# Kernel tuning notes

Measured on AMD Instinct MI355X. Metric: run time of the kernel, lower is better.

The kernel has to match this reference:

```python
import jax, jax.numpy as jnp
import numpy as np

NUM_INSTANCES = 64  # instance ids in [0, 64); id 0 is background and excluded


def _variance_smooth_loss(variances, ins_labels, num_segments):
    # variances: [N, D] float, ins_labels: [N] int
    N, D = variances.shape
    ones = jnp.ones((N,), dtype=variances.dtype)
    counts = jax.ops.segment_sum(ones, ins_labels, num_segments=num_segments)          # [S]
    sums = jax.ops.segment_sum(variances, ins_labels, num_segments=num_segments)       # [S, D]
    safe_counts = jnp.maximum(counts, 1.0)
    means = sums / safe_counts[:, None]                                                # per-instance mean [S, D]
    diff = variances - means[ins_labels]                                               # gather means back [N, D]
    sq = jnp.sum(diff * diff, axis=1)                                                  # [N]
    # per-instance MSE = sum of squared diffs / (K_i * D), matching nn.MSELoss (mean reduction)
    per_ins = jax.ops.segment_sum(sq, ins_labels, num_segments=num_segments) / (safe_counts * D)
    valid = (counts > 0) & (jnp.arange(num_segments) != 0)                             # skip id 0 & absent ids
    return jnp.sum(jnp.where(valid, per_ins, jnp.zeros_like(per_ins)))


def setup_inputs() -> dict:
    key = jax.random.key(0)
    k1, k2 = jax.random.split(key)
    N, D = 4_000_000, 8
    variances = jax.random.normal(k1, (N, D), dtype=jnp.float32)
    ins_labels = jax.random.randint(k2, (N,), 0, NUM_INSTANCES, dtype=jnp.int32)
    return {"variances": variances, "ins_labels": ins_labels}


def reference(variances, ins_labels):
    return _variance_smooth_loss(variances, ins_labels, NUM_INSTANCES)
```

## Files before the change

### kernel.cpp

```cpp
#include <hip/hip_runtime.h>

#define NUM_INST 64
#define SLOT 12
#define BLOCK 256
#define NWAVES 4
#define GRID 1024

__global__ __launch_bounds__(BLOCK) void vsl_main(const float4* __restrict__ rows,
                                                  const int* __restrict__ labels,
                                                  float* __restrict__ gacc, int n) {
    __shared__ float lds[NWAVES][NUM_INST * SLOT];
    const int tid = threadIdx.x;
    const int w = tid >> 6;
    const int lane = tid & 63;

    float s0 = 0, s1 = 0, s2 = 0, s3 = 0, s4 = 0, s5 = 0, s6 = 0, s7 = 0;
    float ssq = 0, cntf = 0;

    float* slotbase = &lds[w][lane * SLOT];
    const int stride = GRID * BLOCK;

    for (int i = blockIdx.x * BLOCK + tid;; i += stride) {
        const bool valid = (i < n);
        const unsigned long long bv = __ballot(valid);
        if (!bv) break;

        int lbl = 0;
        float4 a = {0, 0, 0, 0}, b = {0, 0, 0, 0};
        if (valid) {
            lbl = labels[i];
            a = rows[2 * i];
            b = rows[2 * i + 1];
        }

        *(float4*)(slotbase) = a;
        *(float4*)(slotbase + 4) = b;

        unsigned long long m = bv;
#pragma unroll
        for (int bpos = 0; bpos < 6; ++bpos) {
            const unsigned long long bb = __ballot((lbl >> bpos) & 1);
            m &= ((lane >> bpos) & 1) ? bb : ~bb;
        }
        cntf += (float)__popcll(m);

        asm volatile("s_waitcnt lgkmcnt(0)" ::: "memory");

        while (m) {
            const int s = (int)__builtin_ctzll(m);
            m &= m - 1;
            const float* sp = &lds[w][s * SLOT];
            const float4 p = *(const float4*)sp;
            const float4 q = *(const float4*)(sp + 4);
            s0 += p.x; s1 += p.y; s2 += p.z; s3 += p.w;
            s4 += q.x; s5 += q.y; s6 += q.z; s7 += q.w;
            ssq += p.x * p.x + p.y * p.y + p.z * p.z + p.w * p.w +
                   q.x * q.x + q.y * q.y + q.z * q.z + q.w * q.w;
        }
    }

    float* fb = &lds[w][lane * SLOT];
    fb[0] = s0; fb[1] = s1; fb[2] = s2; fb[3] = s3;
    fb[4] = s4; fb[5] = s5; fb[6] = s6; fb[7] = s7;
    fb[8] = ssq; fb[9] = cntf;
    __syncthreads();

    for (int j = tid; j < NUM_INST * 10; j += BLOCK) {
        const int lbl = j / 10;
        const int st = j - lbl * 10;
        float v = 0;
#pragma unroll
        for (int ww = 0; ww < NWAVES; ++ww) v += lds[ww][lbl * SLOT + st];
        atomicAdd(&gacc[j], v);
    }
}

__global__ __launch_bounds__(64) void vsl_final(const float* __restrict__ gacc,
                                                float* __restrict__ out) {
    const int s = threadIdx.x;
    float val = 0.0f;
    const float* base = &gacc[s * 10];
    const float cnt = base[9];
    if (s != 0 && cnt > 0.0f) {
        const float ss = base[8];
        float m2 = 0.0f;
#pragma unroll
        for (int d = 0; d < 8; ++d) {
            const float sd = base[d];
            m2 += sd * sd;
        }
        val = (ss - m2 / cnt) / (cnt * 8.0f);
    }
#pragma unroll
    for (int off = 32; off > 0; off >>= 1) val += __shfl_down(val, off, 64);
    if (s == 0) out[0] = val;
}

extern "C" void kernel_launch(void* const* d_in, const int* in_sizes, int n_in,
                              void* d_out, int out_size, void* d_ws, size_t ws_size,
                              hipStream_t stream) {
    const float* variances = (const float*)d_in[0];
    const int* labels = (const int*)d_in[1];
    const int n = in_sizes[1];
    float* gacc = (float*)d_ws;

    hipMemsetAsync(d_ws, 0, NUM_INST * 10 * sizeof(float), stream);
    vsl_main<<<GRID, BLOCK, 0, stream>>>((const float4*)variances, labels, gacc, n);
    vsl_final<<<1, 64, 0, stream>>>(gacc, (float*)d_out);
}
```

Baseline: 211.6 us.

## Prefetch next rows, precompute squares per row, use packed FP32 math and divergent slot scan

The main loop now software-pipelines the global loads, issuing the next iteration's label and row loads before processing the current one. Each lane computes its own row's squared norm once with packed FMA and publishes it to LDS, so the gather loop only adds a scalar instead of recomputing eight squares. Accumulation uses v_pk_add_f32 on paired channels, the lane-mask scan uses per-lane 32-bit find-first-bit, and the grid grows to 1792 blocks. The prefetch raises register pressure, and the extra LDS slot plus the per-lane loop adds some complexity.

```diff
diff --git a/kernel.cpp b/kernel.cpp
--- a/kernel.cpp
+++ b/kernel.cpp
@@ -2,39 +2,63 @@
 
 #define NUM_INST 64
 #define SLOT 12
+#define NSLOT 65
 #define BLOCK 256
 #define NWAVES 4
-#define GRID 1024
+#define GRID 1792
 
-__global__ __launch_bounds__(BLOCK) void vsl_main(const float4* __restrict__ rows,
+typedef float f32x4 __attribute__((ext_vector_type(4)));
+typedef float f32x2 __attribute__((ext_vector_type(2)));
+
+__device__ __forceinline__ void pk_add(f32x2& acc, f32x2 v) {
+    asm("v_pk_add_f32 %0, %0, %1" : "+v"(acc) : "v"(v));
+}
+__device__ __forceinline__ void pk_fma_sq(f32x2& acc, f32x2 v) {
+    asm("v_pk_fma_f32 %0, %1, %1, %0" : "+v"(acc) : "v"(v));
+}
+
+__global__ __launch_bounds__(BLOCK) void vsl_main(const f32x4* __restrict__ rows,
                                                   const int* __restrict__ labels,
                                                   float* __restrict__ gacc, int n) {
-    __shared__ float lds[NWAVES][NUM_INST * SLOT];
+    __shared__ float lds[NWAVES][NSLOT * SLOT];
     const int tid = threadIdx.x;
     const int w = tid >> 6;
     const int lane = tid & 63;
+    float* const wbase = &lds[w][0];
 
-    float s0 = 0, s1 = 0, s2 = 0, s3 = 0, s4 = 0, s5 = 0, s6 = 0, s7 = 0;
+    if (lane < 9) wbase[64 * SLOT + lane] = 0.0f;
+
+    f32x2 acc01 = {0, 0}, acc23 = {0, 0}, acc45 = {0, 0}, acc67 = {0, 0};
     float ssq = 0, cntf = 0;
 
-    float* slotbase = &lds[w][lane * SLOT];
+    float* const pub = wbase + lane * SLOT;
     const int stride = GRID * BLOCK;
 
-    for (int i = blockIdx.x * BLOCK + tid;; i += stride) {
-        const bool valid = (i < n);
-        const unsigned long long bv = __ballot(valid);
-        if (!bv) break;
+    int i = blockIdx.x * BLOCK + tid;
+    bool valid = (i < n);
+    unsigned long long bv = __ballot(valid);
+    int lbl = 0;
+    f32x4 a = {0, 0, 0, 0}, b = {0, 0, 0, 0};
+    if (valid) { lbl = labels[i]; a = rows[2 * i]; b = rows[2 * i + 1]; }
 
-        int lbl = 0;
-        float4 a = {0, 0, 0, 0}, b = {0, 0, 0, 0};
-        if (valid) {
-            lbl = labels[i];
-            a = rows[2 * i];
-            b = rows[2 * i + 1];
-        }
+    while (bv) {
+        const int inext = i + stride;
+        const bool vnext = (inext < n);
+        const unsigned long long bvn = __ballot(vnext);
+        int lbln = 0;
+        f32x4 an = {0, 0, 0, 0}, bn = {0, 0, 0, 0};
+        if (vnext) { lbln = labels[inext]; an = rows[2 * inext]; bn = rows[2 * inext + 1]; }
 
-        *(float4*)(slotbase) = a;
-        *(float4*)(slotbase + 4) = b;
+        f32x2 sq2 = {0, 0};
+        pk_fma_sq(sq2, __builtin_shufflevector(a, a, 0, 1));
+        pk_fma_sq(sq2, __builtin_shufflevector(a, a, 2, 3));
+        pk_fma_sq(sq2, __builtin_shufflevector(b, b, 0, 1));
+        pk_fma_sq(sq2, __builtin_shufflevector(b, b, 2, 3));
+        const float sq = sq2.x + sq2.y;
+
+        *(f32x4*)pub = a;
+        *(f32x4*)(pub + 4) = b;
+        pub[8] = sq;
 
         unsigned long long m = bv;
 #pragma unroll
@@ -44,33 +68,47 @@
         }
         cntf += (float)__popcll(m);
 
+        unsigned mlo = (unsigned)m;
+        unsigned mhi = (unsigned)(m >> 32);
+
         asm volatile("s_waitcnt lgkmcnt(0)" ::: "memory");
 
-        while (m) {
-            const int s = (int)__builtin_ctzll(m);
-            m &= m - 1;
-            const float* sp = &lds[w][s * SLOT];
-            const float4 p = *(const float4*)sp;
-            const float4 q = *(const float4*)(sp + 4);
-            s0 += p.x; s1 += p.y; s2 += p.z; s3 += p.w;
-            s4 += q.x; s5 += q.y; s6 += q.z; s7 += q.w;
-            ssq += p.x * p.x + p.y * p.y + p.z * p.z + p.w * p.w +
-                   q.x * q.x + q.y * q.y + q.z * q.z + q.w * q.w;
+        while (mlo | mhi) {
+            unsigned slo, shi;
+            asm("v_ffbl_b32 %0, %1" : "=v"(slo) : "v"(mlo));
+            asm("v_ffbl_b32 %0, %1" : "=v"(shi) : "v"(mhi));
+            const unsigned s = min(slo, min(shi, 32u) + 32u);
+            const bool uselo = (mlo != 0);
+            const unsigned nlo = mlo & (mlo - 1);
+            const unsigned nhi = mhi & (mhi - 1);
+            mlo = nlo;
+            mhi = uselo ? mhi : nhi;
+            const float* sp = wbase + s * SLOT;
+            const f32x4 p = *(const f32x4*)sp;
+            const f32x4 q = *(const f32x4*)(sp + 4);
+            const float r = sp[8];
+            pk_add(acc01, __builtin_shufflevector(p, p, 0, 1));
+            pk_add(acc23, __builtin_shufflevector(p, p, 2, 3));
+            pk_add(acc45, __builtin_shufflevector(q, q, 0, 1));
+            pk_add(acc67, __builtin_shufflevector(q, q, 2, 3));
+            ssq += r;
         }
+
+        i = inext; bv = bvn; lbl = lbln; a = an; b = bn;
     }
 
-    float* fb = &lds[w][lane * SLOT];
-    fb[0] = s0; fb[1] = s1; fb[2] = s2; fb[3] = s3;
-    fb[4] = s4; fb[5] = s5; fb[6] = s6; fb[7] = s7;
+    float* fb = wbase + lane * SLOT;
+    fb[0] = acc01.x; fb[1] = acc01.y; fb[2] = acc23.x; fb[3] = acc23.y;
+    fb[4] = acc45.x; fb[5] = acc45.y; fb[6] = acc67.x; fb[7] = acc67.y;
     fb[8] = ssq; fb[9] = cntf;
     __syncthreads();
 
     for (int j = tid; j < NUM_INST * 10; j += BLOCK) {
-        const int lbl = j / 10;
-        const int st = j - lbl * 10;
+        const int L = j / 10;
+        const int st = j - L * 10;
         float v = 0;
 #pragma unroll
-        for (int ww = 0; ww < NWAVES; ++ww) v += lds[ww][lbl * SLOT + st];
+        for (int ww = 0; ww < NWAVES; ++ww) v += lds[ww][L * SLOT + st];
         atomicAdd(&gacc[j], v);
     }
 }
@@ -105,6 +143,6 @@
     float* gacc = (float*)d_ws;
 
     hipMemsetAsync(d_ws, 0, NUM_INST * 10 * sizeof(float), stream);
-    vsl_main<<<GRID, BLOCK, 0, stream>>>((const float4*)variances, labels, gacc, n);
+    vsl_main<<<GRID, BLOCK, 0, stream>>>((const f32x4*)variances, labels, gacc, n);
     vsl_final<<<1, 64, 0, stream>>>(gacc, (float*)d_out);
 }
```

Measured after the change: 223.8 us. 1.06x slower.

## Compute per-instance segment sums with bf16 MFMA one-hot matmuls

Applied to the files above, without the earlier changes.

Replaces the ballot-based label matching and LDS serial accumulation with a one-hot label matrix multiplied on MFMA 16x16x32 bf16 units. Each value is split into a hi/lo bf16 pair to keep near-fp32 accuracy, and squares are accumulated in a second MFMA. The grid size is also doubled. This removes the per-wave serial loop over matching lanes but adds bf16 split error and per-element conversion cost. Loads become per-float rather than float4, so coalescing changes.

```diff
diff --git a/kernel.cpp b/kernel.cpp
--- a/kernel.cpp
+++ b/kernel.cpp
@@ -1,76 +1,124 @@
 #include <hip/hip_runtime.h>
 
 #define NUM_INST 64
-#define SLOT 12
 #define BLOCK 256
 #define NWAVES 4
-#define GRID 1024
+#define GRID 2048
 
-__global__ __launch_bounds__(BLOCK) void vsl_main(const float4* __restrict__ rows,
+typedef float f32x4 __attribute__((ext_vector_type(4)));
+typedef short s16x8 __attribute__((ext_vector_type(8)));
+typedef int   i32x4 __attribute__((ext_vector_type(4)));
+
+union FragU { i32x4 i; s16x8 s; };
+
+__device__ __forceinline__ unsigned hilo_pack(float v) {
+    unsigned h, p;
+    asm("v_cvt_pk_bf16_f32 %0, %1, %1" : "=v"(h) : "v"(v));
+    const float r = v - __uint_as_float(h << 16);
+    asm("v_cvt_pk_bf16_f32 %0, %1, %2" : "=v"(p) : "v"(v), "v"(r));
+    return p;
+}
+
+__global__ __launch_bounds__(BLOCK) void vsl_main(const float* __restrict__ rows,
                                                   const int* __restrict__ labels,
                                                   float* __restrict__ gacc, int n) {
-    __shared__ float lds[NWAVES][NUM_INST * SLOT];
     const int tid = threadIdx.x;
     const int w = tid >> 6;
     const int lane = tid & 63;
+    const int g = lane >> 4;
+    const int c = lane & 15;
+    const int cc = c & 7;
 
-    float s0 = 0, s1 = 0, s2 = 0, s3 = 0, s4 = 0, s5 = 0, s6 = 0, s7 = 0;
-    float ssq = 0, cntf = 0;
+    f32x4 accS[4], accQ[4];
+#pragma unroll
+    for (int t = 0; t < 4; ++t) { accS[t] = (f32x4){0,0,0,0}; accQ[t] = (f32x4){0,0,0,0}; }
 
-    float* slotbase = &lds[w][lane * SLOT];
-    const int stride = GRID * BLOCK;
+    const int waveId = blockIdx.x * NWAVES + w;
+    const int nWavesTot = GRID * NWAVES;
+    const int nChunks = (n + 15) >> 4;
 
-    for (int i = blockIdx.x * BLOCK + tid;; i += stride) {
-        const bool valid = (i < n);
-        const unsigned long long bv = __ballot(valid);
-        if (!bv) break;
+    for (int ch = waveId; ch < nChunks; ch += nWavesTot) {
+        const int base = ch << 4;
+        const int r0 = base + 2 * g;
+        unsigned b1[4], b2[4];
+        int lbl[4];
 
-        int lbl = 0;
-        float4 a = {0, 0, 0, 0}, b = {0, 0, 0, 0};
-        if (valid) {
-            lbl = labels[i];
-            a = rows[2 * i];
-            b = rows[2 * i + 1];
+        if (base + 16 <= n) {
+            const int2 lp = *(const int2*)(labels + r0);
+            const int2 lq = *(const int2*)(labels + r0 + 8);
+            lbl[0] = lp.x; lbl[1] = lp.y; lbl[2] = lq.x; lbl[3] = lq.y;
+            const float v0 = rows[(r0    ) * 8 + cc];
+            const float v1 = rows[(r0 + 1) * 8 + cc];
+            const float v2 = rows[(r0 + 8) * 8 + cc];
+            const float v3 = rows[(r0 + 9) * 8 + cc];
+            if (c < 8) {
+                b1[0] = hilo_pack(v0);      b1[1] = hilo_pack(v1);
+                b1[2] = hilo_pack(v2);      b1[3] = hilo_pack(v3);
+                b2[0] = hilo_pack(v0 * v0); b2[1] = hilo_pack(v1 * v1);
+                b2[2] = hilo_pack(v2 * v2); b2[3] = hilo_pack(v3 * v3);
+            } else {
+                const unsigned one = (c == 8) ? 0x3F80u : 0u;
+                b1[0] = b1[1] = b1[2] = b1[3] = one;
+                b2[0] = b2[1] = b2[2] = b2[3] = 0u;
+            }
+        } else {
+#pragma unroll
+            for (int q = 0; q < 4; ++q) {
+                const int rq = r0 + (q & 1) + ((q >> 1) * 8);
+                const bool ok = rq < n;
+                const int sq = ok ? rq : 0;
+                const float vq = rows[sq * 8 + cc];
+                lbl[q] = ok ? labels[sq] : -1;
+                if (c < 8) {
+                    b1[q] = ok ? hilo_pack(vq) : 0u;
+                    b2[q] = ok ? hilo_pack(vq * vq) : 0u;
+                } else {
+                    b1[q] = (c == 8 && ok) ? 0x3F80u : 0u;
+                    b2[q] = 0u;
+                }
+            }
         }
 
-        *(float4*)(slotbase) = a;
-        *(float4*)(slotbase + 4) = b;
+        FragU B1, B2;
+        B1.i = (i32x4){(int)b1[0], (int)b1[1], (int)b1[2], (int)b1[3]};
+        B2.i = (i32x4){(int)b2[0], (int)b2[1], (int)b2[2], (int)b2[3]};
 
-        unsigned long long m = bv;
 #pragma unroll
-        for (int bpos = 0; bpos < 6; ++bpos) {
-            const unsigned long long bb = __ballot((lbl >> bpos) & 1);
-            m &= ((lane >> bpos) & 1) ? bb : ~bb;
-        }
-        cntf += (float)__popcll(m);
-
-        asm volatile("s_waitcnt lgkmcnt(0)" ::: "memory");
-
-        while (m) {
-            const int s = (int)__builtin_ctzll(m);
-            m &= m - 1;
-            const float* sp = &lds[w][s * SLOT];
-            const float4 p = *(const float4*)sp;
-            const float4 q = *(const float4*)(sp + 4);
-            s0 += p.x; s1 += p.y; s2 += p.z; s3 += p.w;
-            s4 += q.x; s5 += q.y; s6 += q.z; s7 += q.w;
-            ssq += p.x * p.x + p.y * p.y + p.z * p.z + p.w * p.w +
-                   q.x * q.x + q.y * q.y + q.z * q.z + q.w * q.w;
+        for (int t = 0; t < 4; ++t) {
+            const int m = c + 16 * t;
+            FragU A;
+            A.i = (i32x4){ lbl[0] == m ? (int)0x3F803F80 : 0,
+                           lbl[1] == m ? (int)0x3F803F80 : 0,
+                           lbl[2] == m ? (int)0x3F803F80 : 0,
+                           lbl[3] == m ? (int)0x3F803F80 : 0 };
+            accS[t] = __builtin_amdgcn_mfma_f32_16x16x32_bf16(A.s, B1.s, accS[t], 0, 0, 0);
+            accQ[t] = __builtin_amdgcn_mfma_f32_16x16x32_bf16(A.s, B2.s, accQ[t], 0, 0, 0);
         }
     }
 
-    float* fb = &lds[w][lane * SLOT];
-    fb[0] = s0; fb[1] = s1; fb[2] = s2; fb[3] = s3;
-    fb[4] = s4; fb[5] = s5; fb[6] = s6; fb[7] = s7;
-    fb[8] = ssq; fb[9] = cntf;
+    __shared__ float red[NWAVES][NUM_INST][12];
+#pragma unroll
+    for (int t = 0; t < 4; ++t) {
+#pragma unroll
+        for (int rg = 0; rg < 4; ++rg) {
+            const int Lr = 16 * t + 4 * g + rg;
+            const float vS = accS[t][rg];
+            if (c < 10) red[w][Lr][(c < 8) ? c : (c == 8 ? 9 : 11)] = vS;
+            float sq = accQ[t][rg];
+            sq += __shfl_xor(sq, 1, 64);
+            sq += __shfl_xor(sq, 2, 64);
+            sq += __shfl_xor(sq, 4, 64);
+            if (c == 0) red[w][Lr][8] = sq;
+        }
+    }
     __syncthreads();
 
     for (int j = tid; j < NUM_INST * 10; j += BLOCK) {
-        const int lbl = j / 10;
-        const int st = j - lbl * 10;
+        const int Lb = j / 10;
+        const int st = j - Lb * 10;
         float v = 0;
 #pragma unroll
-        for (int ww = 0; ww < NWAVES; ++ww) v += lds[ww][lbl * SLOT + st];
+        for (int ww = 0; ww < NWAVES; ++ww) v += red[ww][Lb][st];
         atomicAdd(&gacc[j], v);
     }
 }
@@ -105,6 +153,6 @@
     float* gacc = (float*)d_ws;
 
     hipMemsetAsync(d_ws, 0, NUM_INST * 10 * sizeof(float), stream);
-    vsl_main<<<GRID, BLOCK, 0, stream>>>((const float4*)variances, labels, gacc, n);
+    vsl_main<<<GRID, BLOCK, 0, stream>>>(variances, labels, gacc, n);
     vsl_final<<<1, 64, 0, stream>>>(gacc, (float*)d_out);
 }
```

After: 241.3 us. 14.1% more time.
